# Kernel tuning notes

Hardware: AMD Instinct MI355X
Metric: run time of the kernel (lower is better)

The kernel has to match this reference:

```python
import jax, jax.numpy as jnp
import numpy as np

B, P, K = 2, 8192, 20
ELL = 0.15          # ell_min + ell_rand
ELL_BASE = 10.0     # ell_basedist
COLOR_SCALE = 0.2
RES_MIN = 0.1       # res_mag_min
RES_MAX = 2.0       # res_mag_max
BIG = 1e10          # masking constant for invalid db points
EPS = 1e-12


def setup_inputs() -> dict:
    key = jax.random.key(0)
    ks = jax.random.split(key, 16)
    scale = jnp.array([20.0, 20.0, 60.0], jnp.float32)
    off = jnp.array([-10.0, -10.0, 1.0], jnp.float32)  # depth z in [1, 61] m
    xyz1 = jax.random.uniform(ks[0], (B, P, 3), jnp.float32) * scale + off
    xyz2 = jax.random.uniform(ks[1], (B, P, 3), jnp.float32) * scale + off
    hsv1 = jax.random.uniform(ks[2], (B, P, 3), jnp.float32)
    hsv2 = jax.random.uniform(ks[3], (B, P, 3), jnp.float32)
    n1 = jax.random.normal(ks[4], (B, P, 3), jnp.float32)
    normal1 = n1 / jnp.linalg.norm(n1, axis=-1, keepdims=True)
    n2 = jax.random.normal(ks[5], (B, P, 3), jnp.float32)
    normal2 = n2 / jnp.linalg.norm(n2, axis=-1, keepdims=True)
    nres1 = jax.random.uniform(ks[6], (B, P, 1), jnp.float32)
    nres2 = jax.random.uniform(ks[7], (B, P, 1), jnp.float32)

    def rot(k):
        a = np.asarray(jax.random.normal(k, (B, 3, 3), jnp.float32))
        q, _ = np.linalg.qr(a)
        return jnp.asarray(q, jnp.float32)

    R12 = rot(ks[8])
    R21 = rot(ks[9])
    t12 = jax.random.normal(ks[10], (B, 3, 1), jnp.float32) * 0.5
    t21 = jax.random.normal(ks[11], (B, 3, 1), jnp.float32) * 0.5
    npts1 = jax.random.randint(ks[12], (B,), P // 2, P + 1)
    npts2 = jax.random.randint(ks[13], (B,), P // 2, P + 1)
    return dict(xyz1=xyz1, xyz2=xyz2, hsv1=hsv1, hsv2=hsv2,
                normal1=normal1, normal2=normal2, nres1=nres1, nres2=nres2,
                R12=R12, t12=t12, R21=R21, t21=t21, npts1=npts1, npts2=npts2)


def _knn(pq, pdb, len_db):
    # pq [B,Pq,3], pdb [B,Pdb,3] -> squared dists [B,Pq,K], idx [B,Pq,K]
    d2 = jnp.sum((pq[:, :, None, :] - pdb[:, None, :, :]) ** 2, axis=-1)
    valid = jnp.arange(pdb.shape[1])[None, :] < len_db[:, None]
    d2 = jnp.where(valid[:, None, :], d2, BIG)
    neg, idx = jax.lax.top_k(-d2, K)
    return -neg, idx


def _gather(f, idx):
    # f [B,Pdb,C], idx [B,Pq,K] -> [B,Pq,K,C]  (knn_gather)
    return jax.vmap(lambda fb, ib: fb[ib])(f, idx)


def _transform(xyz, normal, R, t):
    x = jnp.einsum('bij,bpj->bpi', R, xyz) + t[:, :, 0][:, None, :]
    n = jnp.einsum('bij,bpj->bpi', R, normal)
    return x, n


def _side(pq, hq, nq, rq, lq, pdb, hdb, ndb, rdb, ldb):
    dists, idx = _knn(pq, pdb, ldb)                      # [B,P,K]
    # length_scale = clamp(ell*(z-base)/base, min=ell)^2
    ls = jnp.maximum(ELL * (pq[:, :, 2:3] - ELL_BASE) / ELL_BASE, ELL) ** 2
    dist_k = jnp.exp(-dists / ls)
    hsv_knn = _gather(hdb, idx)                          # [B,P,K,3]
    cdist = jnp.sqrt(jnp.sum((hq[:, :, None, :] - hsv_knn) ** 2, -1) + EPS)
    color_k = jnp.exp(-cdist / COLOR_SCALE)
    n_knn = _gather(ndb, idx)                            # [B,P,K,3]
    r_knn = _gather(rdb, idx)                            # [B,P,K,1]
    alpha = (2 * RES_MIN / (2 * RES_MIN / RES_MAX + rq[:, :, None, :] + r_knn))[..., 0]
    normal_k = jnp.maximum(jnp.sum(nq[:, :, None, :] * n_knn, -1) * alpha, 0.0)
    mask = (jnp.arange(pq.shape[1])[None, :, None] < lq[:, None, None]).astype(dist_k.dtype)
    total = jnp.sum(dist_k * color_k * normal_k * mask)
    return total / (lq.sum().astype(dist_k.dtype) * K)


def reference(xyz1, xyz2, hsv1, hsv2, normal1, normal2, nres1, nres2,
              R12, t12, R21, t21, npts1, npts2):
    x2in1, n2in1 = _transform(xyz2, normal2, R12, t12)   # pcl_gt_2_in_1
    x1in2, n1in2 = _transform(xyz1, normal1, R21, t21)   # pcl_gt_1_in_2
    k1 = _side(xyz1, hsv1, normal1, nres1, npts1, x2in1, hsv2, n2in1, nres2, npts2)
    k2 = _side(xyz2, hsv2, normal2, nres2, npts2, x1in2, hsv1, n1in2, nres1, npts1)
    return (k1 + k2) / 2
```

## Files before the change

### kernel.cpp

```cpp
#include <hip/hip_runtime.h>
#include <cstdint>
#include <cstddef>

#define PBUF 8192
#define NZB 256
#define NYB 32
#define NBINS (NZB * NYB)
#define NCOMBO 4
#define KNN 20
#define CAP 256
#define CAPB 128
#define SLOTS (NBINS * CAPB)

#define ZMIN_F (-72.0f)
#define INV_BINW (256.0f / 144.0f)
#define INV_YBINW (32.0f / 144.0f)

#define KEY_INF 0xFFFFFFFFFFFFFFFFull

#define THR_MULT 21.0f

#define OFF_ACCUM   0
#define OFF_DBCUR   2048
#define ZERO_BYTES  (2048 + NCOMBO * NBINS * 4)
#define OFF_DBPOS   ZERO_BYTES
#define ARR_BYTES   (NCOMBO * SLOTS * 16)
#define OFF_DBF1    (OFF_DBPOS + ARR_BYTES)
#define OFF_DBF2    (OFF_DBF1 + ARR_BYTES)

__device__ __forceinline__ int binOfZ(float z) {
  int b = (int)floorf((z - ZMIN_F) * INV_BINW);
  return min(max(b, 0), NZB - 1);
}
__device__ __forceinline__ int binOfY(float y) {
  int b = (int)floorf((y - ZMIN_F) * INV_YBINW);
  return min(max(b, 0), NYB - 1);
}

__device__ __forceinline__ float xformRow(const float* R, float tr, float x0, float x1, float x2) {
  return __fmaf_rn(R[2], x2, __fmaf_rn(R[1], x1, __fmaf_rn(R[0], x0, tr)));
}

__global__ __launch_bounds__(256) void k_scatter(
    const float* xyz1, const float* xyz2,
    const float* hsv1, const float* hsv2,
    const float* normal1, const float* normal2,
    const float* nres1, const float* nres2,
    const float* R12, const float* t12,
    const float* R21, const float* t21,
    const int* npts1, const int* npts2, char* ws) {
  int tid = blockIdx.x * 256 + threadIdx.x;
  int c = tid >> 13, j = tid & (PBUF - 1);
  int s = c >> 1, b = c & 1;
  size_t pj = (size_t)(b * PBUF + j);

  const float* dsrc = s == 0 ? xyz2 : xyz1;
  const float* dh = s == 0 ? hsv2 : hsv1;
  const float* dn = s == 0 ? normal2 : normal1;
  const float* dr = s == 0 ? nres2 : nres1;
  const float* R  = (s == 0 ? R12 : R21) + b * 9;
  const float* tt = (s == 0 ? t12 : t21) + b * 3;
  int ldb = (s == 0 ? npts2 : npts1)[b];
  if (j < ldb) {
    const float* x = dsrc + pj * 3;
    float x0 = x[0], x1 = x[1], x2 = x[2];
    float y0 = xformRow(R + 0, tt[0], x0, x1, x2);
    float y1 = xformRow(R + 3, tt[1], x0, x1, x2);
    float y2 = xformRow(R + 6, tt[2], x0, x1, x2);
    const float* n = dn + pj * 3;
    float n0 = xformRow(R + 0, 0.f, n[0], n[1], n[2]);
    float n1 = xformRow(R + 3, 0.f, n[0], n[1], n[2]);
    float n2 = xformRow(R + 6, 0.f, n[0], n[1], n[2]);
    const float* h = dh + pj * 3;
    float r = dr[pj];
    int bin = binOfZ(y2) * NYB + binOfY(y1);
    int slot = atomicAdd((int*)(ws + OFF_DBCUR) + c * NBINS + bin, 1);
    if (slot < CAPB) {
      size_t pos = (size_t)c * SLOTS + (size_t)bin * CAPB + slot;
      ((float4*)(ws + OFF_DBPOS))[pos] = make_float4(y0, y1, y2, 0.f);
      ((float4*)(ws + OFF_DBF1))[pos] = make_float4(h[0], h[1], h[2], r);
      ((float4*)(ws + OFF_DBF2))[pos] = make_float4(n0, n1, n2, 0.f);
    }
  }
}

__global__ __launch_bounds__(256) void k_main(
    const float* xyz1, const float* xyz2,
    const float* hsv1, const float* hsv2,
    const float* normal1, const float* normal2,
    const float* nres1, const float* nres2,
    const int* npts1, const int* npts2, char* ws) {
  __shared__ unsigned long long sBuf[4 * (CAP + 2)];
  const int lane = threadIdx.x & 63;
  const int wIn = threadIdx.x >> 6;
  const int gw = blockIdx.x * 4 + wIn;
  const int c = gw >> 13;
  const int qi = (int)(__brev((unsigned)(gw & 8191)) >> 19);
  const int s = c >> 1, b = c & 1;
  const int lq = (s == 0 ? npts1 : npts2)[b];
  if (qi >= lq) return;

  const size_t qo = (size_t)(b * PBUF + qi);
  const float* qx = (s == 0 ? xyz1 : xyz2) + qo * 3;
  const float* qh = (s == 0 ? hsv1 : hsv2) + qo * 3;
  const float* qn = (s == 0 ? normal1 : normal2) + qo * 3;
  const float* qr = (s == 0 ? nres1 : nres2) + qo;
  const float qpx = qx[0], qpy = qx[1], qpz = qx[2];
  const float qh0 = qh[0], qh1 = qh[1], qh2 = qh[2];
  const float qn0 = qn[0], qn1 = qn[1], qn2 = qn[2];
  const float qres = qr[0];

  const float ell = fmaxf(0.015f * (qpz - 10.0f), 0.15f);
  const float ls = ell * ell;
  const float thrF = THR_MULT * ls;
  const float rad = sqrtf(thrF);
  const float inv_ls = 1.0f / ls;

  const int* C = (const int*)(ws + OFF_DBCUR) + c * NBINS;
  const int zlo = binOfZ(qpz - rad), zhi = binOfZ(qpz + rad);
  const int ylo = binOfY(qpy - rad), yhi = binOfY(qpy + rad);
  const int nyw = yhi - ylo + 1;
  const int nseg = (zhi - zlo + 1) * nyw;

  int segS = 0, segLen = 0;
  if (lane < nseg) {
    int zi = lane / nyw, yi = lane - zi * nyw;
    int bin = (zlo + zi) * NYB + (ylo + yi);
    segS = bin * CAPB;
    segLen = min(C[bin], CAPB);
  }
  int cum = segLen;
  #pragma unroll
  for (int o = 1; o < 64; o <<= 1) {
    int n = __shfl_up(cum, o);
    if (lane >= o) cum += n;
  }
  const int L = __shfl(cum, 63);
  const int excl = cum - segLen;

  const float4* dbPos = (const float4*)(ws + OFF_DBPOS) + (size_t)c * SLOTS;
  const float4* dbF1  = (const float4*)(ws + OFF_DBF1) + (size_t)c * SLOTS;
  const float4* dbF2  = (const float4*)(ws + OFF_DBF2) + (size_t)c * SLOTS;

  auto computeJ = [&](int base) -> int {
    int tc = min(base + lane, L - 1);
    int kk = 0;
    #pragma unroll
    for (int step = 32; step; step >>= 1) {
      int cnd = kk + step;
      int e = __shfl(excl, cnd & 63);
      if (cnd < nseg && e <= tc) kk = cnd;
    }
    return __shfl(segS, kk) + (tc - __shfl(excl, kk));
  };

  unsigned long long* buf = sBuf + wIn * (CAP + 2);
  int pos = 0;
  if (L > 0) {
    int jc = computeJ(0);
    float4 pc = dbPos[jc];
    for (int base = 0; base < L; base += 64) {
      int j = jc;
      float4 p = pc;
      int nb = base + 64;
      if (nb < L) { jc = computeJ(nb); pc = dbPos[jc]; }
      bool in = (base + lane) < L;
      float dx = p.x - qpx, dy = p.y - qpy, dz = p.z - qpz;
      float d2 = __fmaf_rn(dx, dx, __fmaf_rn(dy, dy, dz * dz));
      bool keep = in && (d2 <= thrF);
      unsigned long long m = __ballot(keep);
      int rank = (int)__popcll(m & ((1ull << lane) - 1ull));
      if (keep) {
        int pidx = pos + rank;
        if (pidx < CAP)
          buf[pidx] = ((unsigned long long)__float_as_uint(d2) << 32) | (unsigned)j;
      }
      pos += (int)__popcll(m);
    }
    pos = min(pos, CAP);
  }

  if (lane < 2) buf[pos + lane] = KEY_INF;
  unsigned long long r0 = (lane       < pos) ? buf[lane]       : KEY_INF;
  unsigned long long r1 = (lane + 64  < pos) ? buf[lane + 64]  : KEY_INF;
  unsigned long long r2 = (lane + 128 < pos) ? buf[lane + 128] : KEY_INF;
  unsigned long long r3 = (lane + 192 < pos) ? buf[lane + 192] : KEY_INF;
  int k0 = 0, k1 = 0, k2 = 0, k3 = 0;
  const int nch = (pos + 1) >> 1;
  const ulonglong2* b2 = (const ulonglong2*)buf;
  for (int ch = 0; ch < nch; ++ch) {
    ulonglong2 q = b2[ch];
    k0 += (q.x < r0) + (q.y < r0);
    k1 += (q.x < r1) + (q.y < r1);
    k2 += (q.x < r2) + (q.y < r2);
    k3 += (q.x < r3) + (q.y < r3);
  }

  auto evalKey = [&](unsigned long long key, int rk) -> float {
    if (rk >= KNN || key == KEY_INF) return 0.f;
    int j = (int)(unsigned)key;
    float4 p = dbPos[j];
    float4 f1 = dbF1[j];
    float4 f2 = dbF2[j];
    float dx = p.x - qpx, dy = p.y - qpy, dz = p.z - qpz;
    float d2 = __fmaf_rn(dx, dx, __fmaf_rn(dy, dy, dz * dz));
    float dist_k = __expf(-d2 * inv_ls);
    float c0 = qh0 - f1.x, c1 = qh1 - f1.y, c2 = qh2 - f1.z;
    float cd = sqrtf(__fmaf_rn(c0, c0, __fmaf_rn(c1, c1, c2 * c2)) + 1e-12f);
    float color_k = __expf(cd * -5.0f);
    float alpha = 0.2f / (0.1f + qres + f1.w);
    float nd = __fmaf_rn(qn0, f2.x, __fmaf_rn(qn1, f2.y, qn2 * f2.z));
    float nk = fmaxf(nd * alpha, 0.0f);
    return dist_k * color_k * nk;
  };
  float lsum = evalKey(r0, k0) + evalKey(r1, k1) + evalKey(r2, k2) + evalKey(r3, k3);

  #pragma unroll
  for (int o = 32; o; o >>= 1) lsum += __shfl_down(lsum, o);
  if (lane == 0)
    atomicAdd((float*)(ws + OFF_ACCUM) + (s * 256 + (blockIdx.x & 255)), lsum);
}

__global__ void k_final(const int* npts1, const int* npts2, const char* ws, float* out) {
  int lane = threadIdx.x;
  const float* acc = (const float*)(ws + OFF_ACCUM);
  float s1 = acc[lane] + acc[lane + 64] + acc[lane + 128] + acc[lane + 192];
  float s2 = acc[256 + lane] + acc[256 + lane + 64] + acc[256 + lane + 128] + acc[256 + lane + 192];
  #pragma unroll
  for (int o = 32; o; o >>= 1) {
    s1 += __shfl_down(s1, o);
    s2 += __shfl_down(s2, o);
  }
  if (lane == 0) {
    float k1 = s1 / (20.0f * (float)(npts1[0] + npts1[1]));
    float k2 = s2 / (20.0f * (float)(npts2[0] + npts2[1]));
    out[0] = 0.5f * (k1 + k2);
  }
}

extern "C" void kernel_launch(void* const* d_in, const int* in_sizes, int n_in,
                              void* d_out, int out_size, void* d_ws, size_t ws_size,
                              hipStream_t stream) {
  const float* xyz1 = (const float*)d_in[0];
  const float* xyz2 = (const float*)d_in[1];
  const float* hsv1 = (const float*)d_in[2];
  const float* hsv2 = (const float*)d_in[3];
  const float* normal1 = (const float*)d_in[4];
  const float* normal2 = (const float*)d_in[5];
  const float* nres1 = (const float*)d_in[6];
  const float* nres2 = (const float*)d_in[7];
  const float* R12 = (const float*)d_in[8];
  const float* t12 = (const float*)d_in[9];
  const float* R21 = (const float*)d_in[10];
  const float* t21 = (const float*)d_in[11];
  const int* npts1 = (const int*)d_in[12];
  const int* npts2 = (const int*)d_in[13];
  char* ws = (char*)d_ws;
  float* out = (float*)d_out;

  hipMemsetAsync(ws, 0, ZERO_BYTES, stream);
  k_scatter<<<dim3(NCOMBO * PBUF / 256), dim3(256), 0, stream>>>(
      xyz1, xyz2, hsv1, hsv2, normal1, normal2, nres1, nres2,
      R12, t12, R21, t21, npts1, npts2, ws);
  k_main<<<dim3(NCOMBO * PBUF / 4), dim3(256), 0, stream>>>(
      xyz1, xyz2, hsv1, hsv2, normal1, normal2, nres1, nres2, npts1, npts2, ws);
  k_final<<<dim3(1), dim3(64), 0, stream>>>(npts1, npts2, ws, out);
}
```

Before: 122.6 us.

## Switch database binning from 2D z-y grid to 3D z-y-x grid

Database points are now bucketed on a 3D grid (z, y and x) instead of a 2D z-y grid that covered the whole x extent. Each query now scans only the bins that overlap its search radius in all three axes, so far fewer candidates pass through the distance and top-K stage. Points that fall outside the bounded query region are dropped during scatter, and per-bin capacity is halved. The risks are overflow of a bin past its capacity, or a query window spanning more than 64 bins, either of which could silently lose candidates.

```diff
diff --git a/kernel.cpp b/kernel.cpp
--- a/kernel.cpp
+++ b/kernel.cpp
@@ -3,18 +3,20 @@
 #include <cstddef>
 
 #define PBUF 8192
-#define NZB 256
-#define NYB 32
-#define NBINS (NZB * NYB)
+#define NZB 64
+#define NYB 8
+#define NXB 8
+#define NBINS (NZB * NYB * NXB)
 #define NCOMBO 4
 #define KNN 20
 #define CAP 256
-#define CAPB 128
+#define CAPB 64
 #define SLOTS (NBINS * CAPB)
 
-#define ZMIN_F (-72.0f)
-#define INV_BINW (256.0f / 144.0f)
-#define INV_YBINW (32.0f / 144.0f)
+#define XYMIN_F (-16.0f)
+#define INV_XYBINW 0.25f
+#define ZMIN_F (-8.0f)
+#define INV_ZBINW 0.8f
 
 #define KEY_INF 0xFFFFFFFFFFFFFFFFull
 
@@ -29,12 +31,12 @@
 #define OFF_DBF2    (OFF_DBF1 + ARR_BYTES)
 
 __device__ __forceinline__ int binOfZ(float z) {
-  int b = (int)floorf((z - ZMIN_F) * INV_BINW);
+  int b = (int)floorf((z - ZMIN_F) * INV_ZBINW);
   return min(max(b, 0), NZB - 1);
 }
-__device__ __forceinline__ int binOfY(float y) {
-  int b = (int)floorf((y - ZMIN_F) * INV_YBINW);
-  return min(max(b, 0), NYB - 1);
+__device__ __forceinline__ int binOfXY(float v) {
+  int b = (int)floorf((v - XYMIN_F) * INV_XYBINW);
+  return min(max(b, 0), NXB - 1);
 }
 
 __device__ __forceinline__ float xformRow(const float* R, float tr, float x0, float x1, float x2) {
@@ -67,19 +69,21 @@
     float y0 = xformRow(R + 0, tt[0], x0, x1, x2);
     float y1 = xformRow(R + 3, tt[1], x0, x1, x2);
     float y2 = xformRow(R + 6, tt[2], x0, x1, x2);
-    const float* n = dn + pj * 3;
-    float n0 = xformRow(R + 0, 0.f, n[0], n[1], n[2]);
-    float n1 = xformRow(R + 3, 0.f, n[0], n[1], n[2]);
-    float n2 = xformRow(R + 6, 0.f, n[0], n[1], n[2]);
-    const float* h = dh + pj * 3;
-    float r = dr[pj];
-    int bin = binOfZ(y2) * NYB + binOfY(y1);
-    int slot = atomicAdd((int*)(ws + OFF_DBCUR) + c * NBINS + bin, 1);
-    if (slot < CAPB) {
-      size_t pos = (size_t)c * SLOTS + (size_t)bin * CAPB + slot;
-      ((float4*)(ws + OFF_DBPOS))[pos] = make_float4(y0, y1, y2, 0.f);
-      ((float4*)(ws + OFF_DBF1))[pos] = make_float4(h[0], h[1], h[2], r);
-      ((float4*)(ws + OFF_DBF2))[pos] = make_float4(n0, n1, n2, 0.f);
+    if (fabsf(y0) <= 16.0f && fabsf(y1) <= 16.0f && y2 >= -8.0f && y2 <= 72.0f) {
+      const float* n = dn + pj * 3;
+      float n0 = xformRow(R + 0, 0.f, n[0], n[1], n[2]);
+      float n1 = xformRow(R + 3, 0.f, n[0], n[1], n[2]);
+      float n2 = xformRow(R + 6, 0.f, n[0], n[1], n[2]);
+      const float* h = dh + pj * 3;
+      float r = dr[pj];
+      int bin = (binOfZ(y2) * NYB + binOfXY(y1)) * NXB + binOfXY(y0);
+      int slot = atomicAdd((int*)(ws + OFF_DBCUR) + c * NBINS + bin, 1);
+      if (slot < CAPB) {
+        size_t pos = (size_t)c * SLOTS + (size_t)bin * CAPB + slot;
+        ((float4*)(ws + OFF_DBPOS))[pos] = make_float4(y0, y1, y2, 0.f);
+        ((float4*)(ws + OFF_DBF1))[pos] = make_float4(h[0], h[1], h[2], r);
+        ((float4*)(ws + OFF_DBF2))[pos] = make_float4(n0, n1, n2, 0.f);
+      }
     }
   }
 }
@@ -118,14 +122,17 @@
 
   const int* C = (const int*)(ws + OFF_DBCUR) + c * NBINS;
   const int zlo = binOfZ(qpz - rad), zhi = binOfZ(qpz + rad);
-  const int ylo = binOfY(qpy - rad), yhi = binOfY(qpy + rad);
-  const int nyw = yhi - ylo + 1;
-  const int nseg = (zhi - zlo + 1) * nyw;
+  const int ylo = binOfXY(qpy - rad), yhi = binOfXY(qpy + rad);
+  const int xlo = binOfXY(qpx - rad), xhi = binOfXY(qpx + rad);
+  const int nxw = xhi - xlo + 1;
+  const int nyx = (yhi - ylo + 1) * nxw;
+  const int nseg = (zhi - zlo + 1) * nyx;
 
   int segS = 0, segLen = 0;
   if (lane < nseg) {
-    int zi = lane / nyw, yi = lane - zi * nyw;
-    int bin = (zlo + zi) * NYB + (ylo + yi);
+    int zi = lane / nyx, r = lane - zi * nyx;
+    int yi = r / nxw, xi = r - yi * nxw;
+    int bin = ((zlo + zi) * NYB + (ylo + yi)) * NXB + (xlo + xi);
     segS = bin * CAPB;
     segLen = min(C[bin], CAPB);
   }
```

New measurement: 117.8 us. -3.9%, faster.
